# Optimization experiments

Hardware: AMD Instinct MI355X
Metric: run time of the kernel (lower is better)

## Reference

```python
import jax, jax.numpy as jnp
import numpy as np

H = 128   # LSTM hidden
E = 256   # attention embed dim
NH = 4    # heads


def _lstm_dir(x, Wih, Whh, bih, bhh, reverse):
    # x: [L, D] -> hs: [L, H]; torch gate order i,f,g,o
    xg = x @ Wih.T + bih  # [L, 4H]
    if reverse:
        xg = xg[::-1]
    def step(carry, g):
        h, c = carry
        g = g + h @ Whh.T + bhh
        i, f, gg, o = jnp.split(g, 4)
        i = jax.nn.sigmoid(i); f = jax.nn.sigmoid(f)
        gg = jnp.tanh(gg); o = jax.nn.sigmoid(o)
        c = f * c + i * gg
        h = o * jnp.tanh(c)
        return (h, c), h
    init = (jnp.zeros((H,), x.dtype), jnp.zeros((H,), x.dtype))
    _, hs = jax.lax.scan(step, init, xg)
    if reverse:
        hs = hs[::-1]
    return hs


def _bilstm(x, layers):
    h = x
    for (Wif, Whf, bif, bhf, Wib, Whb, bib, bhb) in layers:
        hf = _lstm_dir(h, Wif, Whf, bif, bhf, False)
        hb = _lstm_dir(h, Wib, Whb, bib, bhb, True)
        h = jnp.concatenate([hf, hb], axis=-1)  # [L, 2H]
    return h


def _mha(x, in_w, in_b, out_w, out_b):
    # x: [L, E] (batch of 1, squeezed); torch MultiheadAttention, eval (no dropout)
    L = x.shape[0]
    hd = E // NH
    qkv = x @ in_w.T + in_b
    q, k, v = jnp.split(qkv, 3, axis=-1)
    q = q.reshape(L, NH, hd).transpose(1, 0, 2)
    k = k.reshape(L, NH, hd).transpose(1, 0, 2)
    v = v.reshape(L, NH, hd).transpose(1, 0, 2)
    scores = jnp.einsum('hqd,hkd->hqk', q, k) / np.float32(np.sqrt(hd))
    attn = jax.nn.softmax(scores, axis=-1)
    out = jnp.einsum('hqk,hkd->hqd', attn, v)
    out = out.transpose(1, 0, 2).reshape(L, E) @ out_w.T + out_b
    return out, attn.mean(axis=0)  # avg over heads (torch default)


def _gconv(src, dst, x, W, b, n):
    # DGL GraphConv norm='none': sum over in-neighbors, linear, bias
    agg = jax.ops.segment_sum(x[src], dst, num_segments=n)
    return agg @ W + b


def setup_inputs():
    key = jax.random.key(0)
    ks = iter(jax.random.split(key, 64))
    def rn(shape, s=0.05):
        return jax.random.normal(next(ks), shape, dtype=jnp.float32) * s
    L, N, EDGES = 512, 50000, 600000
    inp = {}
    inp['g_mol'] = jax.random.normal(next(ks), (L, 14), dtype=jnp.float32)
    inp['feat_seq'] = jax.random.normal(next(ks), (N, 128), dtype=jnp.float32)
    inp['smiles_kmer'] = jax.random.normal(next(ks), (638,), dtype=jnp.float32)
    for l, din in ((0, 14), (1, 256)):
        for d in ('f', 'b'):
            inp['l%d%s_Wih' % (l, d)] = rn((4 * H, din))
            inp['l%d%s_Whh' % (l, d)] = rn((4 * H, H))
            inp['l%d%s_bih' % (l, d)] = rn((4 * H,))
            inp['l%d%s_bhh' % (l, d)] = rn((4 * H,))
    inp['fc_w'] = rn((E, 2 * H)); inp['fc_b'] = rn((E,))
    inp['mha_in_w'] = rn((3 * E, E)); inp['mha_in_b'] = rn((3 * E,))
    inp['mha_out_w'] = rn((E, E)); inp['mha_out_b'] = rn((E,))
    inp['gc1_w'] = rn((128, 128)); inp['gc1_b'] = rn((128,))
    inp['gc2_w'] = rn((128, 256)); inp['gc2_b'] = rn((256,))
    inp['fc1_w'] = rn((575, 1150)); inp['fc1_b'] = rn((575,))
    inp['fc2_w'] = rn((256, 575)); inp['fc2_b'] = rn((256,))
    inp['fc3_w'] = rn((64, 256)); inp['fc3_b'] = rn((64,))
    inp['fc4_w'] = rn((1, 64)); inp['fc4_b'] = rn((1,))
    inp['src'] = jax.random.randint(next(ks), (EDGES,), 0, N, dtype=jnp.int32)
    inp['dst'] = jax.random.randint(next(ks), (EDGES,), 0, N, dtype=jnp.int32)
    return inp


def reference(g_mol, feat_seq, smiles_kmer,
              l0f_Wih, l0f_Whh, l0f_bih, l0f_bhh,
              l0b_Wih, l0b_Whh, l0b_bih, l0b_bhh,
              l1f_Wih, l1f_Whh, l1f_bih, l1f_bhh,
              l1b_Wih, l1b_Whh, l1b_bih, l1b_bhh,
              fc_w, fc_b, mha_in_w, mha_in_b, mha_out_w, mha_out_b,
              gc1_w, gc1_b, gc2_w, gc2_b,
              fc1_w, fc1_b, fc2_w, fc2_b, fc3_w, fc3_b, fc4_w, fc4_b,
              src, dst):
    layers = [(l0f_Wih, l0f_Whh, l0f_bih, l0f_bhh, l0b_Wih, l0b_Whh, l0b_bih, l0b_bhh),
              (l1f_Wih, l1f_Whh, l1f_bih, l1f_bhh, l1b_Wih, l1b_Whh, l1b_bih, l1b_bhh)]
    # BiLSTM + self-attention branch on the molecule sequence
    lstm_out = _bilstm(g_mol, layers)              # [L, 2H]
    proj = lstm_out @ fc_w.T + fc_b                # [L, E]
    attn_out, attn_w = _mha(proj, mha_in_w, mha_in_b, mha_out_w, mha_out_b)
    mol_emb = attn_out[-1]                         # last token, [E]
    # Two-layer GCN on the sequence graph + mean_nodes readout
    n = feat_seq.shape[0]
    h = jax.nn.relu(_gconv(src, dst, feat_seq, gc1_w, gc1_b, n))
    h = _gconv(src, dst, h, gc2_w, gc2_b, n)       # [N, 256]
    hg = h.mean(axis=0)                            # [256]
    feats = jnp.concatenate([hg, mol_emb, smiles_kmer])[None, :]  # [1, 1150]
    o = jax.nn.relu(feats @ fc1_w.T + fc1_b)
    o = jax.nn.relu(o @ fc2_w.T + fc2_b)
    o = jax.nn.relu(o @ fc3_w.T + fc3_b)
    o = o @ fc4_w.T + fc4_b                        # [1, 1]
    return o, attn_w[None]                         # ([1,1], [1,L,L])
```

## Files before the change

kernel.cpp:

```cpp
#include <hip/hip_runtime.h>
#include <hip/hip_bf16.h>

#define L 512
#define H 128
#define E 256
#define NN 50000
#define NE 600000

__device__ float g_xg[4][L*512];
__device__ float g_hs[4][L*H];
__device__ float g_proj[L*E];
__device__ float g_qkv[L*3*E];
__device__ float g_kmat[E*L];
__device__ float g_a511[4*L];
__device__ float g_molemb[E];
__device__ float g_ssum[H];
__device__ float g_hg[E];
__device__ float g_agg[NN*H];
__device__ int   g_cnt_dst[NN];
__device__ int   g_cnt_src[NN];
__device__ int   g_offs[NN+1];
__device__ int   g_cursor[NN];
__device__ int   g_eidx[NE];

__device__ __forceinline__ float sigm(float x){ return 1.f/(1.f+__expf(-x)); }
__device__ __forceinline__ float tanh_f(float x){ float e=__expf(2.f*x); return 1.f - 2.f/(e+1.f); }

__global__ void zero_kernel(){
  int i = blockIdx.x*blockDim.x + threadIdx.x;
  if (i < NN){ g_cnt_dst[i]=0; g_cnt_src[i]=0; }
  if (i < H) g_ssum[i]=0.f;
}

__global__ void hist_kernel(const int* __restrict__ src, const int* __restrict__ dst){
  int i = blockIdx.x*blockDim.x + threadIdx.x;
  if (i < NE){
    atomicAdd(&g_cnt_dst[dst[i]], 1);
    atomicAdd(&g_cnt_src[src[i]], 1);
  }
}

__global__ __launch_bounds__(1024) void scan_kernel(){
  __shared__ int part[1024];
  const int t = threadIdx.x;
  const int CH = 49;
  const int base = t*CH;
  int s = 0;
  for (int i=0;i<CH;i++){ int v=base+i; if (v<NN) s += g_cnt_dst[v]; }
  part[t] = s;
  __syncthreads();
  for (int off=1; off<1024; off<<=1){
    int v = part[t];
    if (t >= off) v += part[t-off];
    __syncthreads();
    part[t] = v;
    __syncthreads();
  }
  int run = part[t] - s;
  for (int i=0;i<CH;i++){
    int v = base+i;
    if (v < NN){ g_offs[v]=run; g_cursor[v]=run; run += g_cnt_dst[v]; }
  }
  if (t == 1023) g_offs[NN] = part[1023];
}

__global__ void fill_kernel(const int* __restrict__ src, const int* __restrict__ dst){
  int i = blockIdx.x*blockDim.x + threadIdx.x;
  if (i < NE){
    int p = atomicAdd(&g_cursor[dst[i]], 1);
    g_eidx[p] = src[i];
  }
}

__global__ __launch_bounds__(64) void agg_kernel(const float* __restrict__ feat){
  const int v = blockIdx.x;
  const int t = threadIdx.x;
  const int s = g_offs[v], e = g_offs[v+1];
  float2 acc = make_float2(0.f, 0.f);
  for (int j=s; j<e; ++j){
    const int sv = g_eidx[j];
    float2 x = ((const float2*)(feat + sv*H))[t];
    acc.x += x.x; acc.y += x.y;
  }
  ((float2*)(g_agg + v*H))[t] = acc;
}

__global__ __launch_bounds__(256) void gemm1_kernel(const float* __restrict__ W, const float* __restrict__ b){
  __shared__ __align__(16) float ash[8*H];
  const int tid = threadIdx.x;
  const int base = blockIdx.x * 8;
  for (int i=tid; i<8*H; i+=256) ash[i] = g_agg[base*H + i];
  __syncthreads();
  const int r  = tid >> 5;
  const int j4 = tid & 31;
  float4 acc = ((const float4*)b)[j4];
  const float* arow = ash + r*H;
  const float4* W4 = (const float4*)W;
  #pragma unroll 8
  for (int k=0;k<H;++k){
    float4 wv = W4[k*32 + j4];
    float av = arow[k];
    acc.x += av*wv.x; acc.y += av*wv.y; acc.z += av*wv.z; acc.w += av*wv.w;
  }
  float4 o = make_float4(fmaxf(acc.x,0.f), fmaxf(acc.y,0.f), fmaxf(acc.z,0.f), fmaxf(acc.w,0.f));
  ((float4*)(g_agg + (base + r)*H))[j4] = o;
}

__global__ __launch_bounds__(128) void wsum_kernel(){
  const int c = threadIdx.x;
  const int v0 = blockIdx.x * 98;
  const int v1 = (v0+98 < NN) ? v0+98 : NN;
  float acc = 0.f;
  for (int v=v0; v<v1; ++v)
    acc += (float)g_cnt_src[v] * g_agg[v*H + c];
  atomicAdd(&g_ssum[c], acc);
}

__global__ __launch_bounds__(256) void hg_kernel(const float* __restrict__ W2, const float* __restrict__ b2){
  __shared__ float ssh[H];
  const int j = threadIdx.x;
  if (j < H) ssh[j] = g_ssum[j] * (1.f/(float)NN);
  __syncthreads();
  float acc = b2[j];
  #pragma unroll 8
  for (int k=0;k<H;++k) acc += ssh[k]*W2[k*E + j];
  g_hg[j] = acc;
}

__global__ __launch_bounds__(512) void xg0_kernel(const float* __restrict__ x,
    const float* __restrict__ Wf, const float* __restrict__ bif, const float* __restrict__ bhf,
    const float* __restrict__ Wb, const float* __restrict__ bib, const float* __restrict__ bhb){
  const int t = blockIdx.x, dir = blockIdx.y, j = threadIdx.x;
  __shared__ float xr[14];
  if (j < 14) xr[j] = x[t*14 + j];
  __syncthreads();
  const float* W = dir ? Wb : Wf;
  float acc = dir ? (bib[j]+bhb[j]) : (bif[j]+bhf[j]);
  #pragma unroll
  for (int k=0;k<14;++k) acc += xr[k]*W[j*14 + k];
  g_xg[dir][t*512 + j] = acc;
}

__global__ __launch_bounds__(512) void xg1_kernel(
    const float* __restrict__ Wf, const float* __restrict__ bif, const float* __restrict__ bhf,
    const float* __restrict__ Wb, const float* __restrict__ bib, const float* __restrict__ bhb){
  const int t = blockIdx.x, dir = blockIdx.y, j = threadIdx.x;
  __shared__ __align__(16) float y[E];
  if (j < H) y[j] = g_hs[0][t*H + j];
  else if (j < E) y[j] = g_hs[1][t*H + (j-H)];
  __syncthreads();
  const float* W = dir ? Wb : Wf;
  float acc = dir ? (bib[j]+bhb[j]) : (bif[j]+bhf[j]);
  const float4* w4 = (const float4*)(W + j*E);
  const float4* y4 = (const float4*)y;
  #pragma unroll 8
  for (int k4=0;k4<64;++k4){
    float4 w = w4[k4], p = y4[k4];
    acc += w.x*p.x + w.y*p.y + w.z*p.z + w.w*p.w;
  }
  g_xg[2+dir][t*512 + j] = acc;
}

__global__ __launch_bounds__(512) void lstm_kernel(const float* __restrict__ WhhF,
                                                   const float* __restrict__ WhhB, int layer){
  const int dir = blockIdx.x;
  const float* __restrict__ Whh = dir ? WhhB : WhhF;
  const float* __restrict__ xg  = g_xg[layer*2 + dir];
  float* __restrict__ hs        = g_hs[layer*2 + dir];
  const int j = threadIdx.x;
  float w[H];
  {
    const float4* W4 = (const float4*)(Whh + j*H);
    #pragma unroll
    for (int k4=0;k4<32;++k4){
      float4 v = W4[k4];
      w[4*k4]=v.x; w[4*k4+1]=v.y; w[4*k4+2]=v.z; w[4*k4+3]=v.w;
    }
  }
  __shared__ __align__(16) float hsm[H];
  __shared__ float gates[512];
  if (j < H) hsm[j] = 0.f;
  float c = 0.f;
  __syncthreads();
  const int gate = j >> 7;
  int tt0 = dir ? (L-1) : 0;
  float xg_cur = xg[tt0*512 + j];
  for (int t=0; t<L; ++t){
    const int tt = dir ? (L-1-t) : t;
    int ttn = dir ? (L-2-t) : (t+1);
    ttn = ttn < 0 ? 0 : (ttn > L-1 ? L-1 : ttn);
    const float xg_next = xg[ttn*512 + j];
    float acc = xg_cur;
    const float4* h4 = (const float4*)hsm;
    #pragma unroll
    for (int k4=0;k4<32;++k4){
      float4 hv = h4[k4];
      acc += w[4*k4]*hv.x + w[4*k4+1]*hv.y + w[4*k4+2]*hv.z + w[4*k4+3]*hv.w;
    }
    float a = (gate == 2) ? tanh_f(acc) : sigm(acc);
    gates[j] = a;
    __syncthreads();
    if (j < H){
      c = gates[H+j]*c + gates[j]*gates[2*H+j];
      float hn = gates[3*H+j]*tanh_f(c);
      hsm[j] = hn;
      hs[tt*H + j] = hn;
    }
    __syncthreads();
    xg_cur = xg_next;
  }
}

__global__ __launch_bounds__(256) void proj_kernel(const float* __restrict__ fcw, const float* __restrict__ fcb){
  const int t = blockIdx.x, j = threadIdx.x;
  __shared__ __align__(16) float y[E];
  y[j] = (j < H) ? g_hs[2][t*H + j] : g_hs[3][t*H + (j-H)];
  __syncthreads();
  float acc = fcb[j];
  const float4* w4 = (const float4*)(fcw + j*E);
  const float4* y4 = (const float4*)y;
  #pragma unroll 8
  for (int k4=0;k4<64;++k4){
    float4 w = w4[k4], p = y4[k4];
    acc += w.x*p.x + w.y*p.y + w.z*p.z + w.w*p.w;
  }
  g_proj[t*E + j] = acc;
}

__global__ __launch_bounds__(256) void qkv_kernel(const float* __restrict__ inw, const float* __restrict__ inb){
  const int t = blockIdx.x, tid = threadIdx.x;
  __shared__ __align__(16) float pr[E];
  pr[tid] = g_proj[t*E + tid];
  __syncthreads();
  const float4* p4 = (const float4*)pr;
  for (int r=0;r<3;++r){
    const int j = r*E + tid;
    float acc = inb[j];
    const float4* w4 = (const float4*)(inw + j*E);
    #pragma unroll 8
    for (int k4=0;k4<64;++k4){
      float4 w = w4[k4], p = p4[k4];
      acc += w.x*p.x + w.y*p.y + w.z*p.z + w.w*p.w;
    }
    g_qkv[t*3*E + j] = acc;
  }
}

__global__ __launch_bounds__(256) void ktrans_kernel(){
  const int u = blockIdx.x, i = threadIdx.x;
  g_kmat[i*L + u] = g_qkv[u*3*E + E + i];
}

__global__ __launch_bounds__(512) void attn_kernel(float* __restrict__ out){
  const int t = blockIdx.x, u = threadIdx.x;
  const int lane = u & 63, wid = u >> 6;
  __shared__ float qsh[64];
  __shared__ float redm[8], reds[8];
  float accm = 0.f;
  for (int h=0; h<4; ++h){
    __syncthreads();
    if (u < 64) qsh[u] = g_qkv[t*3*E + h*64 + u];
    __syncthreads();
    const float* km = g_kmat + h*64*L + u;
    float s = 0.f;
    #pragma unroll 8
    for (int d=0; d<64; ++d) s += qsh[d]*km[d*L];
    s *= 0.125f;
    float m = s;
    for (int o=32;o;o>>=1) m = fmaxf(m, __shfl_xor(m, o, 64));
    if (lane == 0) redm[wid] = m;
    __syncthreads();
    m = redm[0];
    #pragma unroll
    for (int w2=1;w2<8;++w2) m = fmaxf(m, redm[w2]);
    float e = __expf(s - m);
    float sum = e;
    for (int o=32;o;o>>=1) sum += __shfl_xor(sum, o, 64);
    if (lane == 0) reds[wid] = sum;
    __syncthreads();
    sum = reds[0];
    #pragma unroll
    for (int w2=1;w2<8;++w2) sum += reds[w2];
    float a = e / sum;
    accm += 0.25f * a;
    if (t == L-1) g_a511[h*L + u] = a;
  }
  out[1 + t*L + u] = accm;
}

__global__ __launch_bounds__(256) void head_kernel(const float* __restrict__ ow, const float* __restrict__ ob){
  __shared__ float ash[4*L];
  __shared__ float osh[E];
  const int tid = threadIdx.x;
  for (int i=tid; i<4*L; i+=256) ash[i] = g_a511[i];
  __syncthreads();
  const int h = tid >> 6, d = tid & 63;
  float o = 0.f;
  const float* vp = g_qkv + 2*E + h*64 + d;
  for (int uu=0; uu<L; ++uu) o += ash[h*L + uu]*vp[uu*3*E];
  osh[tid] = o;
  __syncthreads();
  float m = ob[tid];
  const float* w = ow + tid*E;
  #pragma unroll 8
  for (int c2=0;c2<E;++c2) m += osh[c2]*w[c2];
  g_molemb[tid] = m;
}

__global__ __launch_bounds__(640) void mlp_kernel(const float* __restrict__ smiles,
    const float* __restrict__ w1, const float* __restrict__ b1,
    const float* __restrict__ w2, const float* __restrict__ b2,
    const float* __restrict__ w3, const float* __restrict__ b3,
    const float* __restrict__ w4, const float* __restrict__ b4,
    float* __restrict__ out){
  __shared__ float f_sh[1152];
  __shared__ float a1[576];
  __shared__ float a2[256];
  __shared__ float a3[64];
  const int tid = threadIdx.x;
  if (tid < 256) f_sh[tid] = g_hg[tid];
  else if (tid < 512) f_sh[tid] = g_molemb[tid-256];
  if (tid < 638) f_sh[512 + tid] = smiles[tid];
  __syncthreads();
  if (tid < 575){
    float acc = b1[tid];
    const float2* w = (const float2*)(w1 + tid*1150);
    #pragma unroll 5
    for (int k=0;k<575;++k){ float2 wv = w[k]; acc += f_sh[2*k]*wv.x + f_sh[2*k+1]*wv.y; }
    a1[tid] = fmaxf(acc, 0.f);
  }
  __syncthreads();
  if (tid < 256){
    float acc = b2[tid];
    const float* w = w2 + tid*575;
    #pragma unroll 5
    for (int k=0;k<575;++k) acc += a1[k]*w[k];
    a2[tid] = fmaxf(acc, 0.f);
  }
  __syncthreads();
  if (tid < 64){
    float acc = b3[tid];
    const float* w = w3 + tid*256;
    #pragma unroll 8
    for (int k=0;k<256;++k) acc += a2[k]*w[k];
    a3[tid] = fmaxf(acc, 0.f);
  }
  __syncthreads();
  if (tid == 0){
    float acc = b4[0];
    #pragma unroll
    for (int k=0;k<64;++k) acc += a3[k]*w4[k];
    out[0] = acc;
  }
}

extern "C" void kernel_launch(void* const* d_in, const int* in_sizes, int n_in,
                              void* d_out, int out_size, void* d_ws, size_t ws_size,
                              hipStream_t stream){
  (void)in_sizes; (void)n_in; (void)out_size; (void)d_ws; (void)ws_size;
  const float* g_mol   = (const float*)d_in[0];
  const float* feat    = (const float*)d_in[1];
  const float* smiles  = (const float*)d_in[2];
  const float* l0fWih  = (const float*)d_in[3];
  const float* l0fWhh  = (const float*)d_in[4];
  const float* l0fbih  = (const float*)d_in[5];
  const float* l0fbhh  = (const float*)d_in[6];
  const float* l0bWih  = (const float*)d_in[7];
  const float* l0bWhh  = (const float*)d_in[8];
  const float* l0bbih  = (const float*)d_in[9];
  const float* l0bbhh  = (const float*)d_in[10];
  const float* l1fWih  = (const float*)d_in[11];
  const float* l1fWhh  = (const float*)d_in[12];
  const float* l1fbih  = (const float*)d_in[13];
  const float* l1fbhh  = (const float*)d_in[14];
  const float* l1bWih  = (const float*)d_in[15];
  const float* l1bWhh  = (const float*)d_in[16];
  const float* l1bbih  = (const float*)d_in[17];
  const float* l1bbhh  = (const float*)d_in[18];
  const float* fcw     = (const float*)d_in[19];
  const float* fcb     = (const float*)d_in[20];
  const float* inw     = (const float*)d_in[21];
  const float* inb     = (const float*)d_in[22];
  const float* ow      = (const float*)d_in[23];
  const float* ob      = (const float*)d_in[24];
  const float* gc1w    = (const float*)d_in[25];
  const float* gc1b    = (const float*)d_in[26];
  const float* gc2w    = (const float*)d_in[27];
  const float* gc2b    = (const float*)d_in[28];
  const float* w1      = (const float*)d_in[29];
  const float* b1      = (const float*)d_in[30];
  const float* w2      = (const float*)d_in[31];
  const float* b2      = (const float*)d_in[32];
  const float* w3      = (const float*)d_in[33];
  const float* b3      = (const float*)d_in[34];
  const float* w4      = (const float*)d_in[35];
  const float* b4      = (const float*)d_in[36];
  const int*   src     = (const int*)d_in[37];
  const int*   dst     = (const int*)d_in[38];
  float* out = (float*)d_out;

  zero_kernel<<<196, 256, 0, stream>>>();
  hist_kernel<<<(NE+255)/256, 256, 0, stream>>>(src, dst);
  scan_kernel<<<1, 1024, 0, stream>>>();
  fill_kernel<<<(NE+255)/256, 256, 0, stream>>>(src, dst);
  agg_kernel<<<NN, 64, 0, stream>>>(feat);
  gemm1_kernel<<<NN/8, 256, 0, stream>>>(gc1w, gc1b);
  wsum_kernel<<<512, 128, 0, stream>>>();
  hg_kernel<<<1, 256, 0, stream>>>(gc2w, gc2b);

  xg0_kernel<<<dim3(L,2), 512, 0, stream>>>(g_mol, l0fWih, l0fbih, l0fbhh, l0bWih, l0bbih, l0bbhh);
  lstm_kernel<<<2, 512, 0, stream>>>(l0fWhh, l0bWhh, 0);
  xg1_kernel<<<dim3(L,2), 512, 0, stream>>>(l1fWih, l1fbih, l1fbhh, l1bWih, l1bbih, l1bbhh);
  lstm_kernel<<<2, 512, 0, stream>>>(l1fWhh, l1bWhh, 1);

  proj_kernel<<<L, 256, 0, stream>>>(fcw, fcb);
  qkv_kernel<<<L, 256, 0, stream>>>(inw, inb);
  ktrans_kernel<<<L, 256, 0, stream>>>();
  attn_kernel<<<L, 512, 0, stream>>>(out);
  head_kernel<<<1, 256, 0, stream>>>(ow, ob);

  mlp_kernel<<<1, 640, 0, stream>>>(smiles, w1, b1, w2, b2, w3, b3, w4, b4, out);
}
```

Before: 1.863 ms.

## Split LSTM recurrence across k-quarters and batch four timesteps in dense kernels

The LSTM step kernel now has each thread compute partial dot products for all four gates over a quarter of the hidden vector. Partials are reduced through shared memory, and one thread per hidden unit applies the gate nonlinearities, with barriers that wait only on LDS. The xg1, proj and qkv kernels each process four timesteps per block so every weight load is reused four times. The K transpose is tiled through shared memory and also emits a transposed V, so the head kernel reads V contiguously with float4. The aim is to shorten the serial recurrence step and to cut redundant weight traffic in the per-timestep GEMVs.

Measured after the change: 1.614 ms. -13.4%, faster.

```diff
diff --git a/kernel.cpp b/kernel.cpp
--- a/kernel.cpp
+++ b/kernel.cpp
@@ -12,6 +12,7 @@
 __device__ float g_proj[L*E];
 __device__ float g_qkv[L*3*E];
 __device__ float g_kmat[E*L];
+__device__ float g_vmat[E*L];
 __device__ float g_a511[4*L];
 __device__ float g_molemb[E];
 __device__ float g_ssum[H];
@@ -26,6 +27,12 @@
 __device__ __forceinline__ float sigm(float x){ return 1.f/(1.f+__expf(-x)); }
 __device__ __forceinline__ float tanh_f(float x){ float e=__expf(2.f*x); return 1.f - 2.f/(e+1.f); }
 
+__device__ __forceinline__ void bar_lds(){
+  asm volatile("s_waitcnt lgkmcnt(0)" ::: "memory");
+  __builtin_amdgcn_s_barrier();
+  __builtin_amdgcn_sched_barrier(0);
+}
+
 __global__ void zero_kernel(){
   int i = blockIdx.x*blockDim.x + threadIdx.x;
   if (i < NN){ g_cnt_dst[i]=0; g_cnt_src[i]=0; }
@@ -144,21 +151,30 @@
 __global__ __launch_bounds__(512) void xg1_kernel(
     const float* __restrict__ Wf, const float* __restrict__ bif, const float* __restrict__ bhf,
     const float* __restrict__ Wb, const float* __restrict__ bib, const float* __restrict__ bhb){
-  const int t = blockIdx.x, dir = blockIdx.y, j = threadIdx.x;
-  __shared__ __align__(16) float y[E];
-  if (j < H) y[j] = g_hs[0][t*H + j];
-  else if (j < E) y[j] = g_hs[1][t*H + (j-H)];
+  const int t0 = blockIdx.x*4, dir = blockIdx.y, j = threadIdx.x;
+  __shared__ __align__(16) float y[4][E];
+  for (int idx=j; idx<4*E; idx+=512){
+    int tl = idx >> 8, c = idx & 255;
+    y[tl][c] = (c < H) ? g_hs[0][(t0+tl)*H + c] : g_hs[1][(t0+tl)*H + (c-H)];
+  }
   __syncthreads();
   const float* W = dir ? Wb : Wf;
-  float acc = dir ? (bib[j]+bhb[j]) : (bif[j]+bhf[j]);
+  float b = dir ? (bib[j]+bhb[j]) : (bif[j]+bhf[j]);
+  float a0=b, a1=b, a2=b, a3=b;
   const float4* w4 = (const float4*)(W + j*E);
-  const float4* y4 = (const float4*)y;
-  #pragma unroll 8
+  #pragma unroll 4
   for (int k4=0;k4<64;++k4){
-    float4 w = w4[k4], p = y4[k4];
-    acc += w.x*p.x + w.y*p.y + w.z*p.z + w.w*p.w;
-  }
-  g_xg[2+dir][t*512 + j] = acc;
+    float4 w = w4[k4];
+    float4 p0=((const float4*)y[0])[k4], p1=((const float4*)y[1])[k4];
+    float4 p2=((const float4*)y[2])[k4], p3=((const float4*)y[3])[k4];
+    a0 += w.x*p0.x + w.y*p0.y + w.z*p0.z + w.w*p0.w;
+    a1 += w.x*p1.x + w.y*p1.y + w.z*p1.z + w.w*p1.w;
+    a2 += w.x*p2.x + w.y*p2.y + w.z*p2.z + w.w*p2.w;
+    a3 += w.x*p3.x + w.y*p3.y + w.z*p3.z + w.w*p3.w;
+  }
+  float* o = g_xg[2+dir];
+  o[(t0+0)*512 + j] = a0; o[(t0+1)*512 + j] = a1;
+  o[(t0+2)*512 + j] = a2; o[(t0+3)*512 + j] = a3;
 }
 
 __global__ __launch_bounds__(512) void lstm_kernel(const float* __restrict__ WhhF,
@@ -167,88 +183,139 @@
   const float* __restrict__ Whh = dir ? WhhB : WhhF;
   const float* __restrict__ xg  = g_xg[layer*2 + dir];
   float* __restrict__ hs        = g_hs[layer*2 + dir];
-  const int j = threadIdx.x;
-  float w[H];
+  const int t = threadIdx.x;
+  const int u = t & 127, q = t >> 7;
+  float wreg[4][32];
+  #pragma unroll
+  for (int g=0; g<4; ++g){
+    const float4* W4 = (const float4*)(Whh + (g*128+u)*H + q*32);
+    #pragma unroll
+    for (int k4=0;k4<8;++k4){
+      float4 v = W4[k4];
+      wreg[g][4*k4]=v.x; wreg[g][4*k4+1]=v.y; wreg[g][4*k4+2]=v.z; wreg[g][4*k4+3]=v.w;
+    }
+  }
+  __shared__ __align__(16) float hsm[H];
+  __shared__ float part[4*512];
+  if (t < H) hsm[t] = 0.f;
+  float c = 0.f;
+  float xgi=0.f, xgf=0.f, xgg=0.f, xgo=0.f;
   {
-    const float4* W4 = (const float4*)(Whh + j*H);
-    #pragma unroll
-    for (int k4=0;k4<32;++k4){
-      float4 v = W4[k4];
-      w[4*k4]=v.x; w[4*k4+1]=v.y; w[4*k4+2]=v.z; w[4*k4+3]=v.w;
-    }
-  }
-  __shared__ __align__(16) float hsm[H];
-  __shared__ float gates[512];
-  if (j < H) hsm[j] = 0.f;
-  float c = 0.f;
-  __syncthreads();
-  const int gate = j >> 7;
-  int tt0 = dir ? (L-1) : 0;
-  float xg_cur = xg[tt0*512 + j];
-  for (int t=0; t<L; ++t){
-    const int tt = dir ? (L-1-t) : t;
-    int ttn = dir ? (L-2-t) : (t+1);
-    ttn = ttn < 0 ? 0 : (ttn > L-1 ? L-1 : ttn);
-    const float xg_next = xg[ttn*512 + j];
-    float acc = xg_cur;
-    const float4* h4 = (const float4*)hsm;
-    #pragma unroll
-    for (int k4=0;k4<32;++k4){
-      float4 hv = h4[k4];
-      acc += w[4*k4]*hv.x + w[4*k4+1]*hv.y + w[4*k4+2]*hv.z + w[4*k4+3]*hv.w;
-    }
-    float a = (gate == 2) ? tanh_f(acc) : sigm(acc);
-    gates[j] = a;
-    __syncthreads();
-    if (j < H){
-      c = gates[H+j]*c + gates[j]*gates[2*H+j];
-      float hn = gates[3*H+j]*tanh_f(c);
-      hsm[j] = hn;
-      hs[tt*H + j] = hn;
-    }
-    __syncthreads();
-    xg_cur = xg_next;
+    int tt0 = dir ? (L-1) : 0;
+    if (t < 128){
+      xgi = xg[tt0*512 + u];       xgf = xg[tt0*512 + 128 + u];
+      xgg = xg[tt0*512 + 256 + u]; xgo = xg[tt0*512 + 384 + u];
+    }
+  }
+  __syncthreads();
+  for (int s=0; s<L; ++s){
+    const int tt = dir ? (L-1-s) : s;
+    float hq[32];
+    const float4* h4 = (const float4*)(hsm + q*32);
+    #pragma unroll
+    for (int k4=0;k4<8;++k4){
+      float4 v = h4[k4];
+      hq[4*k4]=v.x; hq[4*k4+1]=v.y; hq[4*k4+2]=v.z; hq[4*k4+3]=v.w;
+    }
+    float a0=0.f, a1=0.f, a2=0.f, a3=0.f;
+    #pragma unroll
+    for (int k=0;k<32;++k){
+      float hv = hq[k];
+      a0 += wreg[0][k]*hv; a1 += wreg[1][k]*hv;
+      a2 += wreg[2][k]*hv; a3 += wreg[3][k]*hv;
+    }
+    part[q*512 + u]       = a0;
+    part[q*512 + 128 + u] = a1;
+    part[q*512 + 256 + u] = a2;
+    part[q*512 + 384 + u] = a3;
+    bar_lds();
+    if (t < 128){
+      float gi = xgi + part[u]       + part[512+u]       + part[1024+u]       + part[1536+u];
+      float gf = xgf + part[128+u]   + part[640+u]       + part[1152+u]       + part[1664+u];
+      float gg = xgg + part[256+u]   + part[768+u]       + part[1280+u]       + part[1792+u];
+      float go = xgo + part[384+u]   + part[896+u]       + part[1408+u]       + part[1920+u];
+      int ttn = dir ? (L-2-s) : (s+1);
+      ttn = ttn < 0 ? 0 : (ttn > L-1 ? L-1 : ttn);
+      xgi = xg[ttn*512 + u];       xgf = xg[ttn*512 + 128 + u];
+      xgg = xg[ttn*512 + 256 + u]; xgo = xg[ttn*512 + 384 + u];
+      gi = sigm(gi); gf = sigm(gf); gg = tanh_f(gg); go = sigm(go);
+      c = gf*c + gi*gg;
+      float hn = go*tanh_f(c);
+      hsm[u] = hn;
+      hs[tt*H + u] = hn;
+    }
+    bar_lds();
   }
 }
 
 __global__ __launch_bounds__(256) void proj_kernel(const float* __restrict__ fcw, const float* __restrict__ fcb){
-  const int t = blockIdx.x, j = threadIdx.x;
-  __shared__ __align__(16) float y[E];
-  y[j] = (j < H) ? g_hs[2][t*H + j] : g_hs[3][t*H + (j-H)];
-  __syncthreads();
-  float acc = fcb[j];
+  const int t0 = blockIdx.x*4, j = threadIdx.x;
+  __shared__ __align__(16) float y[4][E];
+  for (int idx=j; idx<4*E; idx+=256){
+    int tl = idx >> 8, c = idx & 255;
+    y[tl][c] = (c < H) ? g_hs[2][(t0+tl)*H + c] : g_hs[3][(t0+tl)*H + (c-H)];
+  }
+  __syncthreads();
+  float b = fcb[j];
+  float a0=b, a1=b, a2=b, a3=b;
   const float4* w4 = (const float4*)(fcw + j*E);
-  const float4* y4 = (const float4*)y;
-  #pragma unroll 8
+  #pragma unroll 4
   for (int k4=0;k4<64;++k4){
-    float4 w = w4[k4], p = y4[k4];
-    acc += w.x*p.x + w.y*p.y + w.z*p.z + w.w*p.w;
-  }
-  g_proj[t*E + j] = acc;
+    float4 w = w4[k4];
+    float4 p0=((const float4*)y[0])[k4], p1=((const float4*)y[1])[k4];
+    float4 p2=((const float4*)y[2])[k4], p3=((const float4*)y[3])[k4];
+    a0 += w.x*p0.x + w.y*p0.y + w.z*p0.z + w.w*p0.w;
+    a1 += w.x*p1.x + w.y*p1.y + w.z*p1.z + w.w*p1.w;
+    a2 += w.x*p2.x + w.y*p2.y + w.z*p2.z + w.w*p2.w;
+    a3 += w.x*p3.x + w.y*p3.y + w.z*p3.z + w.w*p3.w;
+  }
+  g_proj[(t0+0)*E + j] = a0; g_proj[(t0+1)*E + j] = a1;
+  g_proj[(t0+2)*E + j] = a2; g_proj[(t0+3)*E + j] = a3;
 }
 
 __global__ __launch_bounds__(256) void qkv_kernel(const float* __restrict__ inw, const float* __restrict__ inb){
-  const int t = blockIdx.x, tid = threadIdx.x;
-  __shared__ __align__(16) float pr[E];
-  pr[tid] = g_proj[t*E + tid];
-  __syncthreads();
-  const float4* p4 = (const float4*)pr;
+  const int t0 = blockIdx.x*4, tid = threadIdx.x;
+  __shared__ __align__(16) float pr[4][E];
+  for (int idx=tid; idx<4*E; idx+=256) pr[idx>>8][idx&255] = g_proj[t0*E + idx];
+  __syncthreads();
   for (int r=0;r<3;++r){
     const int j = r*E + tid;
-    float acc = inb[j];
+    float b = inb[j];
+    float a0=b, a1=b, a2=b, a3=b;
     const float4* w4 = (const float4*)(inw + j*E);
-    #pragma unroll 8
+    #pragma unroll 4
     for (int k4=0;k4<64;++k4){
-      float4 w = w4[k4], p = p4[k4];
-      acc += w.x*p.x + w.y*p.y + w.z*p.z + w.w*p.w;
-    }
-    g_qkv[t*3*E + j] = acc;
+      float4 w = w4[k4];
+      float4 p0=((const float4*)pr[0])[k4], p1=((const float4*)pr[1])[k4];
+      float4 p2=((const float4*)pr[2])[k4], p3=((const float4*)pr[3])[k4];
+      a0 += w.x*p0.x + w.y*p0.y + w.z*p0.z + w.w*p0.w;
+      a1 += w.x*p1.x + w.y*p1.y + w.z*p1.z + w.w*p1.w;
+      a2 += w.x*p2.x + w.y*p2.y + w.z*p2.z + w.w*p2.w;
+      a3 += w.x*p3.x + w.y*p3.y + w.z*p3.z + w.w*p3.w;
+    }
+    g_qkv[(t0+0)*768 + j] = a0; g_qkv[(t0+1)*768 + j] = a1;
+    g_qkv[(t0+2)*768 + j] = a2; g_qkv[(t0+3)*768 + j] = a3;
   }
 }
 
 __global__ __launch_bounds__(256) void ktrans_kernel(){
-  const int u = blockIdx.x, i = threadIdx.x;
-  g_kmat[i*L + u] = g_qkv[u*3*E + E + i];
+  __shared__ float tK[32][33];
+  __shared__ float tV[32][33];
+  const int bu = blockIdx.x, bc = blockIdx.y;
+  const int tx = threadIdx.x & 31, ty = threadIdx.x >> 5;
+  #pragma unroll
+  for (int r=0; r<32; r+=8){
+    int uu = bu*32 + ty + r;
+    tK[ty+r][tx] = g_qkv[uu*768 + 256 + bc*32 + tx];
+    tV[ty+r][tx] = g_qkv[uu*768 + 512 + bc*32 + tx];
+  }
+  __syncthreads();
+  #pragma unroll
+  for (int r=0; r<32; r+=8){
+    int cc = bc*32 + ty + r;
+    g_kmat[cc*512 + bu*32 + tx] = tK[tx][ty+r];
+    g_vmat[cc*512 + bu*32 + tx] = tV[tx][ty+r];
+  }
 }
 
 __global__ __launch_bounds__(512) void attn_kernel(float* __restrict__ out){
@@ -289,15 +356,20 @@
 }
 
 __global__ __launch_bounds__(256) void head_kernel(const float* __restrict__ ow, const float* __restrict__ ob){
-  __shared__ float ash[4*L];
+  __shared__ __align__(16) float ash[4*L];
   __shared__ float osh[E];
   const int tid = threadIdx.x;
   for (int i=tid; i<4*L; i+=256) ash[i] = g_a511[i];
   __syncthreads();
   const int h = tid >> 6, d = tid & 63;
   float o = 0.f;
-  const float* vp = g_qkv + 2*E + h*64 + d;
-  for (int uu=0; uu<L; ++uu) o += ash[h*L + uu]*vp[uu*3*E];
+  const float4* v4 = (const float4*)(g_vmat + (h*64+d)*L);
+  const float4* a4 = (const float4*)(ash + h*L);
+  #pragma unroll 4
+  for (int uu=0; uu<128; ++uu){
+    float4 v = v4[uu], a = a4[uu];
+    o += a.x*v.x + a.y*v.y + a.z*v.z + a.w*v.w;
+  }
   osh[tid] = o;
   __syncthreads();
   float m = ob[tid];
@@ -410,12 +482,12 @@
 
   xg0_kernel<<<dim3(L,2), 512, 0, stream>>>(g_mol, l0fWih, l0fbih, l0fbhh, l0bWih, l0bbih, l0bbhh);
   lstm_kernel<<<2, 512, 0, stream>>>(l0fWhh, l0bWhh, 0);
-  xg1_kernel<<<dim3(L,2), 512, 0, stream>>>(l1fWih, l1fbih, l1fbhh, l1bWih, l1bbih, l1bbhh);
+  xg1_kernel<<<dim3(128,2), 512, 0, stream>>>(l1fWih, l1fbih, l1fbhh, l1bWih, l1bbih, l1bbhh);
   lstm_kernel<<<2, 512, 0, stream>>>(l1fWhh, l1bWhh, 1);
 
-  proj_kernel<<<L, 256, 0, stream>>>(fcw, fcb);
-  qkv_kernel<<<L, 256, 0, stream>>>(inw, inb);
-  ktrans_kernel<<<L, 256, 0, stream>>>();
+  proj_kernel<<<128, 256, 0, stream>>>(fcw, fcb);
+  qkv_kernel<<<128, 256, 0, stream>>>(inw, inb);
+  ktrans_kernel<<<dim3(16,8), 256, 0, stream>>>();
   attn_kernel<<<L, 512, 0, stream>>>(out);
   head_kernel<<<1, 256, 0, stream>>>(ow, ob);
 
```
